# Kernel tuning notes

Measured on AMD Instinct MI355X. Metric: run time of the kernel, lower is better.

The kernel has to match this reference:

```python
import jax, jax.numpy as jnp
import numpy as np

TOP_K = 6
CAP_FACTOR = 2.0


def setup_inputs() -> dict:
    key = jax.random.key(0)
    ks = jax.random.split(key, 9)
    B, S, D, F, E, SH = 4, 2048, 512, 256, 64, 2
    return {
        "x": jax.random.normal(ks[0], (B, S, D), jnp.float32),
        "router_w": jax.random.normal(ks[1], (E, D), jnp.float32) * 0.02,
        "bias": jnp.zeros((E,), jnp.float32),
        "shared_w_gate": jax.random.normal(ks[2], (SH, F, D), jnp.float32) * 0.02,
        "shared_w_up": jax.random.normal(ks[3], (SH, F, D), jnp.float32) * 0.02,
        "shared_w_down": jax.random.normal(ks[4], (SH, D, F), jnp.float32) * 0.02,
        "w_gate": jax.random.normal(ks[5], (E, F, D), jnp.float32) * 0.02,
        "w_up": jax.random.normal(ks[6], (E, F, D), jnp.float32) * 0.02,
        "w_down": jax.random.normal(ks[7], (E, D, F), jnp.float32) * 0.02,
    }


def reference(x, router_w, bias, shared_w_gate, shared_w_up, shared_w_down, w_gate, w_up, w_down):
    B, S, D = x.shape
    E = router_w.shape[0]
    K = TOP_K
    N = B * S
    C = max(1, int(N * K * CAP_FACTOR / E))  # static per-expert capacity

    # Router logits with balancing bias (loop_idx=0 row).
    router_logits = jnp.einsum('bsd,ed->bse', x, router_w) + bias

    # Shared experts: averaged SwiGLU over SH experts, fully batched.
    hg = jnp.einsum('bsd,efd->bsef', x, shared_w_gate)
    hu = jnp.einsum('bsd,efd->bsef', x, shared_w_up)
    shared_out = jnp.einsum('bsef,edf->bsd', jax.nn.silu(hg) * hu, shared_w_down)
    shared_out = shared_out / shared_w_gate.shape[0]

    # Top-k routing, renormalised gates.
    router_probs = jax.nn.softmax(router_logits, axis=-1)
    topk_p, topk_i = jax.lax.top_k(router_probs, K)  # [B,S,K]
    topk_p = topk_p / (jnp.sum(topk_p, axis=-1, keepdims=True) + 1e-9)

    x_flat = x.reshape(N, D)
    flat_e = topk_i.reshape(-1)            # [N*K] expert ids
    flat_g = topk_p.reshape(-1)            # [N*K] gates
    token_ids = jnp.repeat(jnp.arange(N), K)

    # Stable sort by expert id -> contiguous expert groups.
    order = jnp.argsort(flat_e)            # jax argsort is stable
    se = flat_e[order]
    st = token_ids[order]
    sg = flat_g[order]

    M = se.shape[0]
    pos = jnp.arange(M)
    is_first = jnp.concatenate([jnp.ones((1,), bool), se[1:] != se[:-1]])
    group_starts = jax.lax.cummax(pos * is_first.astype(pos.dtype))
    slot = pos - group_starts              # position within expert group
    valid = slot < C                       # capacity drop
    safe_slot = jnp.where(valid, slot, C)  # overflow -> scratch slot C

    # Static-shape dispatch buffers (E, C+1, ...); slot C is scratch.
    expert_in = jnp.zeros((E, C + 1, D), x.dtype).at[se, safe_slot].set(x_flat[st])
    expert_gate = jnp.zeros((E, C + 1), x.dtype).at[se, safe_slot].set(sg)
    expert_tok = jnp.full((E, C + 1), N, jnp.int32).at[se, safe_slot].set(st.astype(jnp.int32))
    expert_mask = jnp.zeros((E, C + 1), bool).at[se, safe_slot].set(valid)

    expert_in = expert_in[:, :C]
    expert_gate = expert_gate[:, :C]
    expert_tok = expert_tok[:, :C]
    expert_mask = expert_mask[:, :C]

    # Grouped SwiGLU: three batched GEMMs over experts.
    hg = jnp.einsum('ecd,efd->ecf', expert_in, w_gate)
    hu = jnp.einsum('ecd,efd->ecf', expert_in, w_up)
    expert_out = jnp.einsum('ecf,edf->ecd', jax.nn.silu(hg) * hu, w_down)

    # Combine: scatter-add gated outputs back to tokens; row N is a sink.
    fm = expert_mask.reshape(-1)
    dst = jnp.where(fm, expert_tok.reshape(-1), N)
    fg = jnp.where(fm, expert_gate.reshape(-1), jnp.zeros((), x.dtype))
    sparse = jax.ops.segment_sum(fg[:, None] * expert_out.reshape(-1, D), dst, num_segments=N + 1)[:N]

    return shared_out + sparse.reshape(B, S, D)
```

## Files before the change

### kernel.cpp

```cpp
#include <hip/hip_runtime.h>
#include <hip/hip_bf16.h>
#include <math.h>

#define N_TOK 8192
#define D_DIM 512
#define F_DIM 256
#define E_NUM 64
#define SH_NUM 2
#define K_TOP 6
#define CAP   1536
#define M_ENT (N_TOK * K_TOP)
#define NCHUNK (M_ENT / 256)

#define EW_STRIDE 393216
#define E_TOT (E_NUM + SH_NUM)
#define X_BF_BYTES   (8388608ull)
#define WT_BYTES     ((size_t)E_TOT * EW_STRIDE * 2)
#define TOK_ROUTED   (E_NUM * CAP)
#define TOK_TOTAL    (TOK_ROUTED + SH_NUM * N_TOK)
#define EO_BYTES     ((size_t)TOK_TOTAL * D_DIM * 2)
#define RWT_BYTES    131072ull

#define SLOT 18432

typedef __attribute__((ext_vector_type(8))) short bf16x8;
typedef __attribute__((ext_vector_type(8))) short short8;
typedef __attribute__((ext_vector_type(4))) float f32x4;

#define VMCNT(n) asm volatile("s_waitcnt vmcnt(" #n ")" ::: "memory")

__device__ __forceinline__ ushort f2bf(float f) {
  union { float f; unsigned u; } c; c.f = f;
  return (ushort)((c.u + 0x7FFFu + ((c.u >> 16) & 1u)) >> 16);
}
__device__ __forceinline__ float bf2f(ushort h) {
  union { unsigned u; float f; } c; c.u = ((unsigned)h) << 16;
  return c.f;
}
__device__ __forceinline__ void gload16(const void* g, void* l) {
  __builtin_amdgcn_global_load_lds(
      (const __attribute__((address_space(1))) void*)g,
      (__attribute__((address_space(3))) void*)l, 16, 0, 0);
}

__global__ void router_topk(const float* __restrict__ x, const float* __restrict__ rw,
                            const float* __restrict__ bias, int* __restrict__ topk_i,
                            float* __restrict__ topk_p) {
  const int wave = threadIdx.x >> 6;
  const int lane = threadIdx.x & 63;
  const int n = blockIdx.x * 4 + wave;
  if (n >= N_TOK) return;

  const float4* xr = (const float4*)(x + (size_t)n * D_DIM);
  const float4* wr = (const float4*)(rw + (size_t)lane * D_DIM);
  float acc = 0.f;
  #pragma unroll 4
  for (int d4 = 0; d4 < D_DIM / 4; ++d4) {
    float4 xv = xr[d4]; float4 wv = wr[d4];
    acc += xv.x * wv.x + xv.y * wv.y + xv.z * wv.z + xv.w * wv.w;
  }
  float logit = acc + bias[lane];

  float m = logit;
  for (int off = 32; off > 0; off >>= 1) m = fmaxf(m, __shfl_xor(m, off));
  float p = expf(logit - m);
  float s = p;
  for (int off = 32; off > 0; off >>= 1) s += __shfl_xor(s, off);
  float prob = p / s;

  float myp = prob;
  float gsum = 0.f;
  float myg = 0.f; int myi = -1;
  for (int k = 0; k < K_TOP; ++k) {
    float bp = myp; int bi = lane;
    for (int off = 32; off > 0; off >>= 1) {
      float op = __shfl_xor(bp, off); int oi = __shfl_xor(bi, off);
      if (op > bp || (op == bp && oi < bi)) { bp = op; bi = oi; }
    }
    gsum += bp;
    if (lane == k) { myg = bp; myi = bi; }
    if (lane == bi) myp = -1.f;
  }
  if (lane < K_TOP) {
    topk_i[n * K_TOP + lane] = myi;
    topk_p[n * K_TOP + lane] = myg / (gsum + 1e-9f);
  }
}

__global__ void transpose_rw(const float* __restrict__ rw, float* __restrict__ rwt) {
  int idx = blockIdx.x * 256 + threadIdx.x;
  if (idx >= E_NUM * (D_DIM / 4)) return;
  int e = idx >> 7, k4 = idx & 127;
  float4 v = *(const float4*)(rw + (size_t)e * D_DIM + k4 * 4);
  *(float4*)(rwt + ((size_t)k4 * 64 + e) * 4) = v;
}

__device__ __forceinline__ void softmax_topk_write(float logit, int n, int lane,
                                                   int* __restrict__ topk_i,
                                                   float* __restrict__ topk_p) {
  float m = logit;
  for (int off = 32; off > 0; off >>= 1) m = fmaxf(m, __shfl_xor(m, off));
  float p = expf(logit - m);
  float s = p;
  for (int off = 32; off > 0; off >>= 1) s += __shfl_xor(s, off);
  float prob = p / s;

  float myp = prob;
  float gsum = 0.f;
  float myg = 0.f; int myi = -1;
  #pragma unroll 1
  for (int k = 0; k < K_TOP; ++k) {
    float bp = myp; int bi = lane;
    for (int off = 32; off > 0; off >>= 1) {
      float op = __shfl_xor(bp, off); int oi = __shfl_xor(bi, off);
      if (op > bp || (op == bp && oi < bi)) { bp = op; bi = oi; }
    }
    gsum += bp;
    if (lane == k) { myg = bp; myi = bi; }
    if (lane == bi) myp = -1.f;
  }
  if (lane < K_TOP) {
    topk_i[n * K_TOP + lane] = myi;
    topk_p[n * K_TOP + lane] = myg / (gsum + 1e-9f);
  }
}

__global__ void __launch_bounds__(256) router_topk2(
    const float* __restrict__ x, const float* __restrict__ rwt,
    const float* __restrict__ bias, int* __restrict__ topk_i,
    float* __restrict__ topk_p) {
  const int wave = threadIdx.x >> 6;
  const int lane = threadIdx.x & 63;
  const int n0 = blockIdx.x * 32 + wave * 8;

  float acc[8];
  #pragma unroll
  for (int t = 0; t < 8; ++t) acc[t] = 0.f;

  const float4* wv4 = (const float4*)rwt;
  #pragma unroll 2
  for (int k4 = 0; k4 < 128; ++k4) {
    float4 w = wv4[k4 * 64 + lane];
    #pragma unroll
    for (int t = 0; t < 8; ++t) {
      float4 xv = *(const float4*)(x + (size_t)(n0 + t) * D_DIM + k4 * 4);
      acc[t] += xv.x * w.x + xv.y * w.y + xv.z * w.z + xv.w * w.w;
    }
  }
  float b = bias[lane];
  #pragma unroll 1
  for (int t = 0; t < 8; ++t)
    softmax_topk_write(acc[t] + b, n0 + t, lane, topk_i, topk_p);
}

__global__ void hist_kernel(const int* __restrict__ topk_i, int* __restrict__ chunk_hist) {
  __shared__ int h[E_NUM];
  const int tid = threadIdx.x;
  if (tid < E_NUM) h[tid] = 0;
  __syncthreads();
  int e = topk_i[blockIdx.x * 256 + tid];
  atomicAdd(&h[e], 1);
  __syncthreads();
  if (tid < E_NUM) chunk_hist[blockIdx.x * E_NUM + tid] = h[tid];
}

__global__ void scan_kernel(const int* __restrict__ chunk_hist, int* __restrict__ chunk_base) {
  const int e = threadIdx.x;
  int run = 0;
  for (int c = 0; c < NCHUNK; ++c) {
    chunk_base[c * E_NUM + e] = run;
    run += chunk_hist[c * E_NUM + e];
  }
}

__global__ void dispatch_kernel(const int* __restrict__ topk_i, const float* __restrict__ topk_p,
                                const int* __restrict__ chunk_base,
                                int* __restrict__ expert_tok, float* __restrict__ expert_gate,
                                int* __restrict__ entry_row) {
  __shared__ int eid[256];
  const int tid = threadIdx.x;
  const int m = blockIdx.x * 256 + tid;
  const int e = topk_i[m];
  eid[tid] = e;
  __syncthreads();
  int rank = 0;
  for (int t = 0; t < tid; ++t) rank += (eid[t] == e);
  int slot = chunk_base[blockIdx.x * E_NUM + e] + rank;
  int row = -1;
  if (slot < CAP) {
    expert_tok[e * CAP + slot] = m / K_TOP;
    expert_gate[e * CAP + slot] = topk_p[m];
    row = e * CAP + slot;
  }
  if (entry_row) entry_row[m] = row;
}


__global__ void convert_x(const float* __restrict__ x, ushort* __restrict__ xb) {
  size_t idx = (size_t)blockIdx.x * 256 + threadIdx.x;
  const float4* s4 = (const float4*)(x + idx * 8);
  float4 v0 = s4[0], v1 = s4[1];
  short8 o;
  o[0] = f2bf(v0.x); o[1] = f2bf(v0.y); o[2] = f2bf(v0.z); o[3] = f2bf(v0.w);
  o[4] = f2bf(v1.x); o[5] = f2bf(v1.y); o[6] = f2bf(v1.z); o[7] = f2bf(v1.w);
  *(short8*)(xb + idx * 8) = o;
}

__global__ void convert_w(const float* __restrict__ wg_, const float* __restrict__ wu_,
                          const float* __restrict__ wd_, const float* __restrict__ swg,
                          const float* __restrict__ swu, const float* __restrict__ swd,
                          ushort* __restrict__ Wt) {
  int e = blockIdx.x / 12;
  int rem = blockIdx.x - e * 12;
  int p = rem >> 2, rb = rem & 3;
  const float* src;
  if (p == 0)      src = (e < E_NUM) ? wg_ + (size_t)e * 131072 : swg + (size_t)(e - E_NUM) * 131072;
  else if (p == 1) src = (e < E_NUM) ? wu_ + (size_t)e * 131072 : swu + (size_t)(e - E_NUM) * 131072;
  else             src = (e < E_NUM) ? wd_ + (size_t)e * 131072 : swd + (size_t)(e - E_NUM) * 131072;
  src += (size_t)rb * 32768;
  ushort* dst = Wt + (size_t)e * EW_STRIDE + (size_t)p * 131072;
  #pragma unroll
  for (int i = 0; i < 16; ++i) {
    int g = threadIdx.x + i * 256;
    const float4* s4 = (const float4*)(src + (size_t)g * 8);
    float4 v0 = s4[0], v1 = s4[1];
    short8 o;
    o[0] = f2bf(v0.x); o[1] = f2bf(v0.y); o[2] = f2bf(v0.z); o[3] = f2bf(v0.w);
    o[4] = f2bf(v1.x); o[5] = f2bf(v1.y); o[6] = f2bf(v1.z); o[7] = f2bf(v1.w);
    size_t L = (size_t)rb * 32768 + (size_t)g * 8;
    size_t d;
    if (p < 2) {
      int n = (int)(L >> 9);
      int k = (int)(L & 511);
      int ci = k >> 5;
      int k8 = (k >> 3) & 3;
      d = (size_t)ci * 8192 + (size_t)(n >> 4) * 512 + k8 * 128 + (n & 15) * 8;
    } else {
      int rd = (int)(L >> 8);
      int np = rd >> 8;
      int n  = rd & 255;
      int col = (int)(L & 255);
      int kc = col >> 5;
      int k8 = (col >> 3) & 3;
      int ci = np * 8 + kc;
      d = (size_t)ci * 8192 + (size_t)(n >> 4) * 512 + k8 * 128 + (n & 15) * 8;
    }
    *(short8*)(dst + d) = o;
  }
}

__global__ void init_shared_tok(int* __restrict__ tok_all, float* __restrict__ gate_all) {
  int i = blockIdx.x * 256 + threadIdx.x;
  tok_all[TOK_ROUTED + i] = i & (N_TOK - 1);
  gate_all[TOK_ROUTED + i] = 0.5f;
}

template <bool GATHER>
__global__ void __launch_bounds__(512, 1) ffn_mfma(
    const ushort* __restrict__ xb, const ushort* __restrict__ Wt,
    const int* __restrict__ tok_all, const float* __restrict__ gate_all,
    float* __restrict__ out, ushort* __restrict__ expert_out) {
  int e, tbase;
  if (blockIdx.x < 2 * (N_TOK / 64)) {
    int sid = blockIdx.x;
    int sh = sid & 1, mt = sid >> 1;
    e = E_NUM + sh;
    tbase = TOK_ROUTED + sh * N_TOK + mt * 64;
  } else {
    int rb = blockIdx.x - 2 * (N_TOK / 64);
    e = rb & (E_NUM - 1);
    int mt = rb >> 6;
    tbase = e * CAP + mt * 64;
    if (tok_all[tbase] < 0) return;
  }
  const ushort* wbase = Wt + (size_t)e * EW_STRIDE;

  __shared__ ushort RING[3 * SLOT];
  __shared__ ushort Act[16384];
  __shared__ int   toks[64];
  __shared__ float gts[64];

  const int tid = threadIdx.x;
  const int lane = tid & 63;
  const int wid = tid >> 6;
  const int wr = wid >> 2;
  const int wc = wid & 3;
  const int rl = lane & 15;
  const int hi = lane >> 4;

  if (tid < 64) {
    int t = tok_all[tbase + tid];
    toks[tid] = t;
    gts[tid] = (t >= 0) ? gate_all[tbase + tid] : 0.f;
  }
  __syncthreads();

  int stok = 0;
  if (wid < 4) { int t = toks[wid * 16 + rl]; stok = (t < 0) ? 0 : t; }
  const ushort* xsrc = xb + (size_t)stok * D_DIM + hi * 8;

  auto stage_gu = [&](int sl, int kc) {
    ushort* dst = RING + sl * SLOT;
    if (wid < 4)
      gload16(xsrc + kc * 32, dst + wid * 512);
    #pragma unroll
    for (int i = 0; i < 2; ++i) {
      int s = wid * 2 + i;
      gload16(wbase + kc * 8192 + s * 512 + lane * 8, dst + 2048 + s * 512);
      gload16(wbase + 131072 + kc * 8192 + s * 512 + lane * 8, dst + 10240 + s * 512);
    }
  };
  auto stage_dn = [&](int sl, int kc) {
    ushort* dst = RING + sl * SLOT;
    #pragma unroll
    for (int i = 0; i < 4; ++i) {
      int s = wid * 4 + i;
      gload16(wbase + 262144 + (s >> 4) * 65536 + kc * 8192 + (s & 15) * 512 + lane * 8,
              dst + s * 512);
    }
  };

  const f32x4 fzero = {0.f, 0.f, 0.f, 0.f};
  f32x4 accg[2][4], accu[2][4];
  #pragma unroll
  for (int ri = 0; ri < 2; ++ri)
    #pragma unroll
    for (int bi = 0; bi < 4; ++bi) { accg[ri][bi] = fzero; accu[ri][bi] = fzero; }

  stage_gu(0, 0); stage_gu(1, 1);
  {
    int sl_c = 0, sl_n = 2;
    #pragma unroll 1
    for (int kc = 0; kc < 16; ++kc) {
      if (kc < 14) { stage_gu(sl_n, kc + 2); sl_n = (sl_n == 2) ? 0 : sl_n + 1; }
      if (kc < 14)      { if (wid < 4) VMCNT(10); else VMCNT(8); }
      else if (kc == 14){ if (wid < 4) VMCNT(5);  else VMCNT(4); }
      else              VMCNT(0);
      __builtin_amdgcn_s_barrier();
      __builtin_amdgcn_sched_barrier(0);
      {
        const ushort* base = RING + sl_c * SLOT;
        bf16x8 a[2], bg[4], bu[4];
        #pragma unroll
        for (int ri = 0; ri < 2; ++ri)
          a[ri] = *(const bf16x8*)(base + (wr * 2 + ri) * 512 + lane * 8);
        #pragma unroll
        for (int bi = 0; bi < 4; ++bi) {
          bg[bi] = *(const bf16x8*)(base + 2048 + (wc * 4 + bi) * 512 + lane * 8);
          bu[bi] = *(const bf16x8*)(base + 10240 + (wc * 4 + bi) * 512 + lane * 8);
        }
        __builtin_amdgcn_s_setprio(1);
        #pragma unroll
        for (int ri = 0; ri < 2; ++ri)
          #pragma unroll
          for (int bi = 0; bi < 4; ++bi) {
            accg[ri][bi] = __builtin_amdgcn_mfma_f32_16x16x32_bf16(a[ri], bg[bi], accg[ri][bi], 0, 0, 0);
            accu[ri][bi] = __builtin_amdgcn_mfma_f32_16x16x32_bf16(a[ri], bu[bi], accu[ri][bi], 0, 0, 0);
          }
        __builtin_amdgcn_s_setprio(0);
      }
      sl_c = (sl_c == 2) ? 0 : sl_c + 1;
      __builtin_amdgcn_s_barrier();
    }
  }

  #pragma unroll
  for (int ri = 0; ri < 2; ++ri)
    #pragma unroll
    for (int bi = 0; bi < 4; ++bi) {
      int st = (wr * 2 + ri) * 8 + wc * 2 + (bi >> 1);
      int base = st * 512 + ((bi & 1) * 2 + (rl >> 3)) * 128 + (rl & 7);
      #pragma unroll
      for (int j = 0; j < 4; ++j) {
        float g = accg[ri][bi][j], u = accu[ri][bi][j];
        Act[base + (hi * 4 + j) * 8] = f2bf(g / (1.f + __expf(-g)) * u);
      }
    }

  f32x4 accd[2][8];
  #pragma unroll
  for (int ri = 0; ri < 2; ++ri)
    #pragma unroll
    for (int bj = 0; bj < 8; ++bj) accd[ri][bj] = fzero;

  stage_dn(0, 0); stage_dn(1, 1);
  asm volatile("s_waitcnt lgkmcnt(0)" ::: "memory");
  __builtin_amdgcn_s_barrier();
  __builtin_amdgcn_sched_barrier(0);
  {
    int sl_c = 0, sl_n = 2;
    #pragma unroll 1
    for (int kc = 0; kc < 8; ++kc) {
      if (kc < 6) { stage_dn(sl_n, kc + 2); sl_n = (sl_n == 2) ? 0 : sl_n + 1; }
      if (kc < 6)       VMCNT(8);
      else if (kc == 6) VMCNT(4);
      else              VMCNT(0);
      __builtin_amdgcn_s_barrier();
      __builtin_amdgcn_sched_barrier(0);
      {
        const ushort* base = RING + sl_c * SLOT;
        bf16x8 a[2], b[8];
        #pragma unroll
        for (int ri = 0; ri < 2; ++ri)
          a[ri] = *(const bf16x8*)(Act + ((wr * 2 + ri) * 8 + kc) * 512 + lane * 8);
        #pragma unroll
        for (int bj = 0; bj < 8; ++bj)
          b[bj] = *(const bf16x8*)(base + (wc * 8 + bj) * 512 + lane * 8);
        __builtin_amdgcn_s_setprio(1);
        #pragma unroll
        for (int ri = 0; ri < 2; ++ri)
          #pragma unroll
          for (int bj = 0; bj < 8; ++bj)
            accd[ri][bj] = __builtin_amdgcn_mfma_f32_16x16x32_bf16(a[ri], b[bj], accd[ri][bj], 0, 0, 0);
        __builtin_amdgcn_s_setprio(0);
      }
      sl_c = (sl_c == 2) ? 0 : sl_c + 1;
      __builtin_amdgcn_s_barrier();
    }
  }

  if (GATHER) {
    #pragma unroll
    for (int ri = 0; ri < 2; ++ri)
      #pragma unroll
      for (int j = 0; j < 4; ++j) {
        int r = wr * 32 + ri * 16 + hi * 4 + j;
        if (toks[r] < 0) continue;
        ushort* erow = expert_out + (size_t)(tbase + r) * D_DIM + wc * 128 + rl;
        #pragma unroll
        for (int bj = 0; bj < 8; ++bj)
          erow[bj * 16] = f2bf(accd[ri][bj][j]);
      }
  } else {
    #pragma unroll
    for (int ri = 0; ri < 2; ++ri)
      #pragma unroll
      for (int j = 0; j < 4; ++j) {
        int r = wr * 32 + ri * 16 + hi * 4 + j;
        int t = toks[r];
        if (t < 0) continue;
        float gt = gts[r];
        float* orow = out + (size_t)t * D_DIM + wc * 128 + rl;
        #pragma unroll
        for (int bj = 0; bj < 8; ++bj)
          atomicAdd(orow + bj * 16, gt * accd[ri][bj][j]);
      }
  }
}

__global__ void __launch_bounds__(256) gather_out(
    const ushort* __restrict__ eo, const int* __restrict__ entry_row,
    const float* __restrict__ topk_p, float* __restrict__ out) {
  const int t = blockIdx.x * 4 + (threadIdx.x >> 6);
  const int lane = threadIdx.x & 63;
  const int base = t * K_TOP;

  float acc[8];
  #pragma unroll
  for (int j = 0; j < 8; ++j) acc[j] = 0.f;

  #pragma unroll
  for (int k = 0; k < K_TOP; ++k) {
    int row = entry_row[base + k];
    if (row >= 0) {
      float g = topk_p[base + k];
      bf16x8 v = *(const bf16x8*)(eo + (size_t)row * D_DIM + lane * 8);
      #pragma unroll
      for (int j = 0; j < 8; ++j) acc[j] += g * bf2f((ushort)v[j]);
    }
  }
  #pragma unroll
  for (int sh = 0; sh < SH_NUM; ++sh) {
    int row = TOK_ROUTED + sh * N_TOK + t;
    bf16x8 v = *(const bf16x8*)(eo + (size_t)row * D_DIM + lane * 8);
    #pragma unroll
    for (int j = 0; j < 8; ++j) acc[j] += 0.5f * bf2f((ushort)v[j]);
  }
  float4* o = (float4*)(out + (size_t)t * D_DIM + lane * 8);
  o[0] = make_float4(acc[0], acc[1], acc[2], acc[3]);
  o[1] = make_float4(acc[4], acc[5], acc[6], acc[7]);
}


__global__ void __launch_bounds__(256, 2) expert_ffn_mfma(
    const float* __restrict__ x, const float* __restrict__ wg_,
    const float* __restrict__ wu_, const float* __restrict__ wd_,
    const int* __restrict__ expert_tok, const float* __restrict__ expert_gate,
    float* __restrict__ out) {
  const int e = blockIdx.x & (E_NUM - 1);
  const int mt = blockIdx.x >> 6;
  const int s0 = mt * 64;
  if (expert_tok[e * CAP + s0] < 0) return;

  __shared__ ushort Xs[64][72];
  __shared__ ushort Ws[256][72];
  __shared__ ushort Act[64][264];
  __shared__ int   toks[64];
  __shared__ float gts[64];

  const int tid = threadIdx.x;
  const int lane = tid & 63;
  const int wid = tid >> 6;
  const int rl = lane & 15;
  const int ko = (lane >> 4) * 8;
  const int rquad = (lane >> 4) * 4;

  if (tid < 64) {
    int t = expert_tok[e * CAP + s0 + tid];
    toks[tid] = t;
    gts[tid] = (t >= 0) ? expert_gate[e * CAP + s0 + tid] : 0.f;
  }
  __syncthreads();

  float4 px[4], pw[16];

  auto loadX = [&](int kb) {
    #pragma unroll
    for (int it = 0; it < 4; ++it) {
      int idx = tid + it * 256;
      int row = idx >> 4, c4 = (idx & 15) << 2;
      int t = toks[row];
      px[it] = (t >= 0) ? *(const float4*)(x + (size_t)t * D_DIM + kb * 64 + c4)
                        : make_float4(0.f, 0.f, 0.f, 0.f);
    }
  };
  auto writeX = [&]() {
    #pragma unroll
    for (int it = 0; it < 4; ++it) {
      int idx = tid + it * 256;
      int row = idx >> 4, c4 = (idx & 15) << 2;
      ushort4 h; h.x = f2bf(px[it].x); h.y = f2bf(px[it].y);
      h.z = f2bf(px[it].z); h.w = f2bf(px[it].w);
      *(ushort4*)&Xs[row][c4] = h;
    }
  };
  auto loadW = [&](const float* src, int ldk, int kb) {
    #pragma unroll
    for (int it = 0; it < 16; ++it) {
      int idx = tid + it * 256;
      int row = idx >> 4, c4 = (idx & 15) << 2;
      pw[it] = *(const float4*)(src + (size_t)row * ldk + kb * 64 + c4);
    }
  };
  auto writeW = [&]() {
    #pragma unroll
    for (int it = 0; it < 16; ++it) {
      int idx = tid + it * 256;
      int row = idx >> 4, c4 = (idx & 15) << 2;
      ushort4 h; h.x = f2bf(pw[it].x); h.y = f2bf(pw[it].y);
      h.z = f2bf(pw[it].z); h.w = f2bf(pw[it].w);
      *(ushort4*)&Ws[row][c4] = h;
    }
  };
  auto compute = [&](const ushort* Ab, int lda, f32x4 (&acc)[4][4]) {
    #pragma unroll
    for (int kk = 0; kk < 2; ++kk) {
      bf16x8 a[4], b[4];
      #pragma unroll
      for (int ri = 0; ri < 4; ++ri)
        a[ri] = *(const bf16x8*)(Ab + (size_t)(ri * 16 + rl) * lda + kk * 32 + ko);
      #pragma unroll
      for (int bi = 0; bi < 4; ++bi)
        b[bi] = *(const bf16x8*)(&Ws[wid * 64 + bi * 16 + rl][kk * 32 + ko]);
      #pragma unroll
      for (int ri = 0; ri < 4; ++ri)
        #pragma unroll
        for (int bi = 0; bi < 4; ++bi)
          acc[ri][bi] = __builtin_amdgcn_mfma_f32_16x16x32_bf16(a[ri], b[bi], acc[ri][bi], 0, 0, 0);
    }
  };

  const f32x4 fzero = {0.f, 0.f, 0.f, 0.f};

  #pragma unroll 1
  for (int which = 0; which < 2; ++which) {
    const float* wsrc = (which == 0 ? wg_ : wu_) + (size_t)e * F_DIM * D_DIM;
    f32x4 acc[4][4];
    #pragma unroll
    for (int ri = 0; ri < 4; ++ri)
      #pragma unroll
      for (int bi = 0; bi < 4; ++bi) acc[ri][bi] = fzero;

    loadX(0); loadW(wsrc, D_DIM, 0);
    writeX(); writeW();
    __syncthreads();
    for (int kb = 0; kb < 8; ++kb) {
      if (kb < 7) { loadX(kb + 1); loadW(wsrc, D_DIM, kb + 1); }
      compute(&Xs[0][0], 72, acc);
      __syncthreads();
      if (kb < 7) { writeX(); writeW(); __syncthreads(); }
    }
    #pragma unroll
    for (int ri = 0; ri < 4; ++ri)
      #pragma unroll
      for (int bi = 0; bi < 4; ++bi)
        #pragma unroll
        for (int j = 0; j < 4; ++j) {
          int r = ri * 16 + rquad + j;
          int c = wid * 64 + bi * 16 + rl;
          if (which == 0) {
            Act[r][c] = f2bf(acc[ri][bi][j]);
          } else {
            float hg = bf2f(Act[r][c]);
            float a = hg / (1.f + __expf(-hg)) * acc[ri][bi][j];
            Act[r][c] = f2bf(a);
          }
        }
    __syncthreads();
  }

  #pragma unroll 1
  for (int np = 0; np < 2; ++np) {
    const float* wsrc = wd_ + ((size_t)e * D_DIM + np * 256) * F_DIM;
    f32x4 acc[4][4];
    #pragma unroll
    for (int ri = 0; ri < 4; ++ri)
      #pragma unroll
      for (int bi = 0; bi < 4; ++bi) acc[ri][bi] = fzero;

    loadW(wsrc, F_DIM, 0); writeW();
    __syncthreads();
    for (int kb = 0; kb < 4; ++kb) {
      if (kb < 3) loadW(wsrc, F_DIM, kb + 1);
      compute(&Act[0][kb * 64], 264, acc);
      __syncthreads();
      if (kb < 3) { writeW(); __syncthreads(); }
    }
    #pragma unroll
    for (int ri = 0; ri < 4; ++ri)
      #pragma unroll
      for (int bi = 0; bi < 4; ++bi)
        #pragma unroll
        for (int j = 0; j < 4; ++j) {
          int r = ri * 16 + rquad + j;
          int t = toks[r];
          if (t >= 0) {
            int c = np * 256 + wid * 64 + bi * 16 + rl;
            atomicAdd(out + (size_t)t * D_DIM + c, gts[r] * acc[ri][bi][j]);
          }
        }
  }
}

__global__ void __launch_bounds__(256, 2) shared_ffn_mfma(
    const float* __restrict__ x, const float* __restrict__ swg,
    const float* __restrict__ swu, const float* __restrict__ swd,
    float* __restrict__ out) {
  const int row0 = blockIdx.x * 32;

  __shared__ ushort Xs[32][72];
  __shared__ ushort Ws[256][72];
  __shared__ ushort Act[32][264];

  const int tid = threadIdx.x;
  const int lane = tid & 63;
  const int wid = tid >> 6;
  const int rl = lane & 15;
  const int ko = (lane >> 4) * 8;
  const int rquad = (lane >> 4) * 4;

  float4 px[2], pw[16];

  auto loadX = [&](int kb) {
    #pragma unroll
    for (int it = 0; it < 2; ++it) {
      int idx = tid + it * 256;
      int row = idx >> 4, c4 = (idx & 15) << 2;
      px[it] = *(const float4*)(x + (size_t)(row0 + row) * D_DIM + kb * 64 + c4);
    }
  };
  auto writeX = [&]() {
    #pragma unroll
    for (int it = 0; it < 2; ++it) {
      int idx = tid + it * 256;
      int row = idx >> 4, c4 = (idx & 15) << 2;
      ushort4 h; h.x = f2bf(px[it].x); h.y = f2bf(px[it].y);
      h.z = f2bf(px[it].z); h.w = f2bf(px[it].w);
      *(ushort4*)&Xs[row][c4] = h;
    }
  };
  auto loadW = [&](const float* src, int ldk, int kb) {
    #pragma unroll
    for (int it = 0; it < 16; ++it) {
      int idx = tid + it * 256;
      int row = idx >> 4, c4 = (idx & 15) << 2;
      pw[it] = *(const float4*)(src + (size_t)row * ldk + kb * 64 + c4);
    }
  };
  auto writeW = [&]() {
    #pragma unroll
    for (int it = 0; it < 16; ++it) {
      int idx = tid + it * 256;
      int row = idx >> 4, c4 = (idx & 15) << 2;
      ushort4 h; h.x = f2bf(pw[it].x); h.y = f2bf(pw[it].y);
      h.z = f2bf(pw[it].z); h.w = f2bf(pw[it].w);
      *(ushort4*)&Ws[row][c4] = h;
    }
  };
  auto compute = [&](const ushort* Ab, int lda, f32x4 (&acc)[2][4]) {
    #pragma unroll
    for (int kk = 0; kk < 2; ++kk) {
      bf16x8 a[2], b[4];
      #pragma unroll
      for (int ri = 0; ri < 2; ++ri)
        a[ri] = *(const bf16x8*)(Ab + (size_t)(ri * 16 + rl) * lda + kk * 32 + ko);
      #pragma unroll
      for (int bi = 0; bi < 4; ++bi)
        b[bi] = *(const bf16x8*)(&Ws[wid * 64 + bi * 16 + rl][kk * 32 + ko]);
      #pragma unroll
      for (int ri = 0; ri < 2; ++ri)
        #pragma unroll
        for (int bi = 0; bi < 4; ++bi)
          acc[ri][bi] = __builtin_amdgcn_mfma_f32_16x16x32_bf16(a[ri], b[bi], acc[ri][bi], 0, 0, 0);
    }
  };

  const f32x4 fzero = {0.f, 0.f, 0.f, 0.f};
  f32x4 accd[2][2][4];
  #pragma unroll
  for (int np = 0; np < 2; ++np)
    #pragma unroll
    for (int ri = 0; ri < 2; ++ri)
      #pragma unroll
      for (int bi = 0; bi < 4; ++bi) accd[np][ri][bi] = fzero;

  #pragma unroll 1
  for (int sh = 0; sh < SH_NUM; ++sh) {
    #pragma unroll 1
    for (int which = 0; which < 2; ++which) {
      const float* wsrc = (which == 0 ? swg : swu) + (size_t)sh * F_DIM * D_DIM;
      f32x4 acc[2][4];
      #pragma unroll
      for (int ri = 0; ri < 2; ++ri)
        #pragma unroll
        for (int bi = 0; bi < 4; ++bi) acc[ri][bi] = fzero;

      loadX(0); loadW(wsrc, D_DIM, 0);
      writeX(); writeW();
      __syncthreads();
      for (int kb = 0; kb < 8; ++kb) {
        if (kb < 7) { loadX(kb + 1); loadW(wsrc, D_DIM, kb + 1); }
        compute(&Xs[0][0], 72, acc);
        __syncthreads();
        if (kb < 7) { writeX(); writeW(); __syncthreads(); }
      }
      #pragma unroll
      for (int ri = 0; ri < 2; ++ri)
        #pragma unroll
        for (int bi = 0; bi < 4; ++bi)
          #pragma unroll
          for (int j = 0; j < 4; ++j) {
            int r = ri * 16 + rquad + j;
            int c = wid * 64 + bi * 16 + rl;
            if (which == 0) {
              Act[r][c] = f2bf(acc[ri][bi][j]);
            } else {
              float hg = bf2f(Act[r][c]);
              float a = hg / (1.f + __expf(-hg)) * acc[ri][bi][j];
              Act[r][c] = f2bf(a);
            }
          }
      __syncthreads();
    }
    #pragma unroll
    for (int np = 0; np < 2; ++np) {
      const float* wsrc = swd + ((size_t)sh * D_DIM + np * 256) * F_DIM;
      loadW(wsrc, F_DIM, 0); writeW();
      __syncthreads();
      for (int kb = 0; kb < 4; ++kb) {
        if (kb < 3) loadW(wsrc, F_DIM, kb + 1);
        compute(&Act[0][kb * 64], 264, accd[np]);
        __syncthreads();
        if (kb < 3) { writeW(); __syncthreads(); }
      }
    }
  }

  #pragma unroll
  for (int np = 0; np < 2; ++np)
    #pragma unroll
    for (int ri = 0; ri < 2; ++ri)
      #pragma unroll
      for (int bi = 0; bi < 4; ++bi)
        #pragma unroll
        for (int j = 0; j < 4; ++j) {
          int r = ri * 16 + rquad + j;
          int c = np * 256 + wid * 64 + bi * 16 + rl;
          out[(size_t)(row0 + r) * D_DIM + c] = 0.5f * accd[np][ri][bi][j];
        }
}

extern "C" void kernel_launch(void* const* d_in, const int* in_sizes, int n_in,
                              void* d_out, int out_size, void* d_ws, size_t ws_size,
                              hipStream_t stream) {
  const float* x    = (const float*)d_in[0];
  const float* rw   = (const float*)d_in[1];
  const float* bias = (const float*)d_in[2];
  const float* swg  = (const float*)d_in[3];
  const float* swu  = (const float*)d_in[4];
  const float* swd  = (const float*)d_in[5];
  const float* wg   = (const float*)d_in[6];
  const float* wu   = (const float*)d_in[7];
  const float* wd   = (const float*)d_in[8];
  float* out = (float*)d_out;

  const size_t small = 2 * (size_t)M_ENT * 4 + (size_t)M_ENT * 4 +
                       2 * (size_t)NCHUNK * E_NUM * 4 + 2 * (size_t)TOK_TOTAL * 4 +
                       RWT_BYTES;
  const size_t need_mid = X_BF_BYTES + WT_BYTES + small;
  const size_t need_big = need_mid + EO_BYTES;

  if (ws_size >= need_mid) {
    const bool gather = (ws_size >= need_big);
    char* ws = (char*)d_ws;
    ushort* x_bf     = (ushort*)ws; ws += X_BF_BYTES;
    ushort* Wt       = (ushort*)ws; ws += WT_BYTES;
    int*   topk_i    = (int*)ws;    ws += (size_t)M_ENT * 4;
    float* topk_p    = (float*)ws;  ws += (size_t)M_ENT * 4;
    int*   entry_row = (int*)ws;    ws += (size_t)M_ENT * 4;
    int*   chunk_hist= (int*)ws;    ws += (size_t)NCHUNK * E_NUM * 4;
    int*   chunk_base= (int*)ws;    ws += (size_t)NCHUNK * E_NUM * 4;
    int*   tok_all   = (int*)ws;    ws += (size_t)TOK_TOTAL * 4;
    float* gate_all  = (float*)ws;  ws += (size_t)TOK_TOTAL * 4;
    float* rwt       = (float*)ws;  ws += RWT_BYTES;
    ushort* eo       = (ushort*)ws;

    transpose_rw<<<32, 256, 0, stream>>>(rw, rwt);
    convert_x<<<2048, 256, 0, stream>>>(x, x_bf);
    convert_w<<<E_TOT * 12, 256, 0, stream>>>(wg, wu, wd, swg, swu, swd, Wt);
    router_topk2<<<256, 256, 0, stream>>>(x, rwt, bias, topk_i, topk_p);
    hipMemsetAsync(tok_all, 0xFF, (size_t)TOK_ROUTED * 4, stream);
    if (!gather) hipMemsetAsync(out, 0, (size_t)out_size * 4, stream);
    hist_kernel<<<NCHUNK, 256, 0, stream>>>(topk_i, chunk_hist);
    scan_kernel<<<1, 64, 0, stream>>>(chunk_hist, chunk_base);
    dispatch_kernel<<<NCHUNK, 256, 0, stream>>>(topk_i, topk_p, chunk_base, tok_all,
                                                gate_all, entry_row);
    init_shared_tok<<<64, 256, 0, stream>>>(tok_all, gate_all);
    const int nblk = 2 * (N_TOK / 64) + (CAP / 64) * E_NUM;
    if (gather) {
      ffn_mfma<true><<<nblk, 512, 0, stream>>>(x_bf, Wt, tok_all, gate_all, out, eo);
      gather_out<<<N_TOK / 4, 256, 0, stream>>>(eo, entry_row, topk_p, out);
    } else {
      ffn_mfma<false><<<nblk, 512, 0, stream>>>(x_bf, Wt, tok_all, gate_all, out, nullptr);
    }
  } else {
    char* ws = (char*)d_ws;
    int*   topk_i      = (int*)ws;   ws += (size_t)M_ENT * 4;
    float* topk_p      = (float*)ws; ws += (size_t)M_ENT * 4;
    int*   chunk_hist  = (int*)ws;   ws += (size_t)NCHUNK * E_NUM * 4;
    int*   chunk_base  = (int*)ws;   ws += (size_t)NCHUNK * E_NUM * 4;
    int*   expert_tok  = (int*)ws;   ws += (size_t)E_NUM * CAP * 4;
    float* expert_gate = (float*)ws; ws += (size_t)E_NUM * CAP * 4;

    router_topk<<<N_TOK / 4, 256, 0, stream>>>(x, rw, bias, topk_i, topk_p);
    hipMemsetAsync(expert_tok, 0xFF, (size_t)E_NUM * CAP * 4, stream);
    hist_kernel<<<NCHUNK, 256, 0, stream>>>(topk_i, chunk_hist);
    scan_kernel<<<1, 64, 0, stream>>>(chunk_hist, chunk_base);
    dispatch_kernel<<<NCHUNK, 256, 0, stream>>>(topk_i, topk_p, chunk_base, expert_tok,
                                                expert_gate, nullptr);
    shared_ffn_mfma<<<N_TOK / 32, 256, 0, stream>>>(x, swg, swu, swd, out);
    expert_ffn_mfma<<<(CAP / 64) * E_NUM, 256, 0, stream>>>(x, wg, wu, wd, expert_tok,
                                                            expert_gate, out);
  }
}
```

Measured before the change: 305.6 us.

## Remap FFN blocks so each XCD owns fixed experts; coalesce weight-convert writes

The FFN kernel's block-to-work mapping is changed so that blocks landing on the same XCD (blockIdx & 7) all serve the same set of experts. Each expert's weights then stay in one XCD's L2 instead of being fetched by all eight. Routed experts are also scheduled ahead of the shared-expert tiles. The weight-conversion kernel now iterates over destination offsets, so its writes are contiguous and its reads are gathered. The new mapping assumes a fixed grid size and a round-robin dispatch of blocks across XCDs.

```diff
diff --git a/kernel.cpp b/kernel.cpp
--- a/kernel.cpp
+++ b/kernel.cpp
@@ -212,39 +212,33 @@
                           ushort* __restrict__ Wt) {
   int e = blockIdx.x / 12;
   int rem = blockIdx.x - e * 12;
-  int p = rem >> 2, rb = rem & 3;
+  int p = rem >> 2, q = rem & 3;
   const float* src;
   if (p == 0)      src = (e < E_NUM) ? wg_ + (size_t)e * 131072 : swg + (size_t)(e - E_NUM) * 131072;
   else if (p == 1) src = (e < E_NUM) ? wu_ + (size_t)e * 131072 : swu + (size_t)(e - E_NUM) * 131072;
   else             src = (e < E_NUM) ? wd_ + (size_t)e * 131072 : swd + (size_t)(e - E_NUM) * 131072;
-  src += (size_t)rb * 32768;
   ushort* dst = Wt + (size_t)e * EW_STRIDE + (size_t)p * 131072;
   #pragma unroll
   for (int i = 0; i < 16; ++i) {
-    int g = threadIdx.x + i * 256;
-    const float4* s4 = (const float4*)(src + (size_t)g * 8);
+    int d = q * 32768 + i * 2048 + threadIdx.x * 8;
+    int ci = d >> 13;
+    int r  = d & 8191;
+    int nt = r >> 9;
+    int rr = r & 511;
+    int k8 = rr >> 7;
+    int n  = nt * 16 + ((rr >> 3) & 15);
+    size_t srcidx;
+    if (p < 2) {
+      srcidx = (size_t)n * 512 + ci * 32 + k8 * 8;
+    } else {
+      int np = ci >> 3, kc = ci & 7;
+      srcidx = (size_t)(np * 256 + n) * 256 + kc * 32 + k8 * 8;
+    }
+    const float4* s4 = (const float4*)(src + srcidx);
     float4 v0 = s4[0], v1 = s4[1];
     short8 o;
     o[0] = f2bf(v0.x); o[1] = f2bf(v0.y); o[2] = f2bf(v0.z); o[3] = f2bf(v0.w);
     o[4] = f2bf(v1.x); o[5] = f2bf(v1.y); o[6] = f2bf(v1.z); o[7] = f2bf(v1.w);
-    size_t L = (size_t)rb * 32768 + (size_t)g * 8;
-    size_t d;
-    if (p < 2) {
-      int n = (int)(L >> 9);
-      int k = (int)(L & 511);
-      int ci = k >> 5;
-      int k8 = (k >> 3) & 3;
-      d = (size_t)ci * 8192 + (size_t)(n >> 4) * 512 + k8 * 128 + (n & 15) * 8;
-    } else {
-      int rd = (int)(L >> 8);
-      int np = rd >> 8;
-      int n  = rd & 255;
-      int col = (int)(L & 255);
-      int kc = col >> 5;
-      int k8 = (col >> 3) & 3;
-      int ci = np * 8 + kc;
-      d = (size_t)ci * 8192 + (size_t)(n >> 4) * 512 + k8 * 128 + (n & 15) * 8;
-    }
     *(short8*)(dst + d) = o;
   }
 }
@@ -261,17 +255,21 @@
     const int* __restrict__ tok_all, const float* __restrict__ gate_all,
     float* __restrict__ out, ushort* __restrict__ expert_out) {
   int e, tbase;
-  if (blockIdx.x < 2 * (N_TOK / 64)) {
-    int sid = blockIdx.x;
-    int sh = sid & 1, mt = sid >> 1;
-    e = E_NUM + sh;
-    tbase = TOK_ROUTED + sh * N_TOK + mt * 64;
-  } else {
-    int rb = blockIdx.x - 2 * (N_TOK / 64);
-    e = rb & (E_NUM - 1);
-    int mt = rb >> 6;
-    tbase = e * CAP + mt * 64;
-    if (tok_all[tbase] < 0) return;
+  {
+    int xcd = blockIdx.x & 7;
+    int j = blockIdx.x >> 3;
+    if (j < 192) {
+      int ec = j / 24;
+      int mt = j - ec * 24;
+      e = ec * 8 + xcd;
+      tbase = e * CAP + mt * 64;
+      if (tok_all[tbase] < 0) return;
+    } else {
+      int s = xcd * 32 + (j - 192);
+      int sh = s & 1, mt = s >> 1;
+      e = E_NUM + sh;
+      tbase = TOK_ROUTED + sh * N_TOK + mt * 64;
+    }
   }
   const ushort* wbase = Wt + (size_t)e * EW_STRIDE;
 
```

Result: faster. 283.8 us (-7.1%).
